# Performance work log

Measured on AMD Instinct MI355X. Metric: run time of the kernel, lower is better.

Reference implementation:

```python
import jax, jax.numpy as jnp
import numpy as np

B, L, D, E, R, NMOD = 8, 2048, 4096, 4, 8, 7

def setup_inputs() -> dict:
    key = jax.random.key(0)
    ks = jax.random.split(key, 8)
    return {
        "x": jax.random.normal(ks[0], (B, L, D), dtype=jnp.float32) * 0.02,
        "expert_scores": jax.random.uniform(ks[1], (B, E), dtype=jnp.float32),
        "W_base": jax.random.normal(ks[2], (D, D), dtype=jnp.float32) * 0.02,
        "b_base": jnp.zeros((D,), dtype=jnp.float32),
        "gating_W": jax.random.normal(ks[3], (D, D), dtype=jnp.float32) * 0.02,
        "W_r": jax.random.normal(ks[4], (NMOD, D), dtype=jnp.float32) * 0.02,
        "lora_A": jax.random.normal(ks[5], (E, R, D), dtype=jnp.float32) * 0.02,
        "lora_B": jax.random.normal(ks[6], (E, D, R), dtype=jnp.float32) * 0.02,
        "module_idx": 0,
        "k": 2,
    }

def _gate_weights(expert_scores, module_prob, k, dtype):
    # rank experts by their random score (descending); Top-K -> weight 1/K
    order = jnp.argsort(-expert_scores, axis=-1)           # [B, E]
    rank = jnp.argsort(order, axis=-1)                     # [B, E] rank of each expert
    k_lo = max(1, k // 2)
    w_hi = (rank < k).astype(dtype) / k                    # prob > 0.5 branch
    w_lo = (rank < k_lo).astype(dtype) / k_lo              # prob <= 0.5 branch
    return jnp.where((module_prob > 0.5)[:, None], w_hi, w_lo)  # [B, E]

def reference(x, expert_scores, W_base, b_base, gating_W, W_r, lora_A, lora_B, module_idx, k):
    # Pooler: last token representation
    pooled = x[:, -1, :]                                   # [B, D]
    # Router: softmax(g(h) W_r) -> per-module probability
    gated = pooled @ gating_W.T                            # [B, D]
    logits = gated @ W_r.T                                 # [B, NMOD]
    probs = jax.nn.softmax(logits, axis=-1)
    module_prob = probs[:, module_idx]                     # [B]
    gate = _gate_weights(expert_scores, module_prob, k, x.dtype)  # [B, E]
    # Base linear projection
    base = x @ W_base.T + b_base                           # [B, L, D]
    # LoRA experts: sum_e gate[b,e] * (x @ A_e^T) @ B_e^T
    t = jnp.einsum('bli,eri->belr', x, lora_A)             # [B, E, L, R]
    lora = jnp.einsum('belr,eor,be->blo', t, lora_B, gate) # [B, L, D]
    return base + lora
```

## Files before the change

### kernel.cpp

```cpp
#include <hip/hip_runtime.h>
#include <hip/hip_bf16.h>


typedef short short8 __attribute__((ext_vector_type(8)));
typedef float f32x4v __attribute__((ext_vector_type(4)));

#define M_DIM 16384
#define N_DIM 4096
#define K_DIM 4160
#define D_DIM 4096
#define NGRP 130

__device__ __forceinline__ unsigned short f2b(float f) {
  unsigned u = __builtin_bit_cast(unsigned, f);
  return (unsigned short)((u + 0x7FFFu + ((u >> 16) & 1u)) >> 16);
}
__device__ __forceinline__ void async_copy16(void* lds, const void* g) {
  __builtin_amdgcn_global_load_lds(
      (const __attribute__((address_space(1))) void*)g,
      (__attribute__((address_space(3))) void*)lds, 16, 0, 0);
}
__device__ __forceinline__ short8 frag_ld(const short* base, int row, int ks, int hi, int lo) {
  return *(const short8*)(&base[row * 64 + (((ks * 4 + hi) ^ (lo & 7)) * 8)]);
}

__global__ __launch_bounds__(256) void cvt_x_k(const float* __restrict__ x,
                                               short* __restrict__ xa) {
  size_t idx = (size_t)blockIdx.x * 256 + threadIdx.x;
  size_t row = idx / 520;
  int cc = (int)(idx % 520);
  short8 o;
  if (cc < 512) {
    const float* src = x + row * (size_t)D_DIM + (size_t)cc * 8;
    float4 a = *(const float4*)(src);
    float4 b = *(const float4*)(src + 4);
    o[0] = (short)f2b(a.x); o[1] = (short)f2b(a.y);
    o[2] = (short)f2b(a.z); o[3] = (short)f2b(a.w);
    o[4] = (short)f2b(b.x); o[5] = (short)f2b(b.y);
    o[6] = (short)f2b(b.z); o[7] = (short)f2b(b.w);
  } else {
#pragma unroll
    for (int t = 0; t < 8; ++t) o[t] = 0;
  }
  *(short8*)(xa + row * (size_t)K_DIM + (size_t)cc * 8) = o;
}

__global__ __launch_bounds__(256) void cvt_w_k(const float* __restrict__ Wb,
                                               const float* __restrict__ lB,
                                               short* __restrict__ wa) {
  size_t idx = (size_t)blockIdx.x * 256 + threadIdx.x;
  size_t row = idx / 520;
  int cc = (int)(idx % 520);
  short8 o;
  if (cc < 512) {
    const float* src = Wb + row * (size_t)D_DIM + (size_t)cc * 8;
    float4 a = *(const float4*)(src);
    float4 b = *(const float4*)(src + 4);
    o[0] = (short)f2b(a.x); o[1] = (short)f2b(a.y);
    o[2] = (short)f2b(a.z); o[3] = (short)f2b(a.w);
    o[4] = (short)f2b(b.x); o[5] = (short)f2b(b.y);
    o[6] = (short)f2b(b.z); o[7] = (short)f2b(b.w);
  } else if (cc < 516) {
    int e = cc - 512;
    const float* src = lB + (size_t)e * (D_DIM * 8) + row * 8;
    float4 a = *(const float4*)(src);
    float4 b = *(const float4*)(src + 4);
    o[0] = (short)f2b(a.x); o[1] = (short)f2b(a.y);
    o[2] = (short)f2b(a.z); o[3] = (short)f2b(a.w);
    o[4] = (short)f2b(b.x); o[5] = (short)f2b(b.y);
    o[6] = (short)f2b(b.z); o[7] = (short)f2b(b.w);
  } else {
#pragma unroll
    for (int t = 0; t < 8; ++t) o[t] = 0;
  }
  *(short8*)(wa + row * (size_t)K_DIM + (size_t)cc * 8) = o;
}

__global__ __launch_bounds__(256) void cvt_la_k(const float* __restrict__ lA,
                                                short* __restrict__ lAb) {
  size_t i = (size_t)blockIdx.x * 256 + threadIdx.x;
  const float* s = lA + i * 8;
  float4 a = *(const float4*)s;
  float4 b = *(const float4*)(s + 4);
  short8 o;
  o[0] = (short)f2b(a.x); o[1] = (short)f2b(a.y);
  o[2] = (short)f2b(a.z); o[3] = (short)f2b(a.w);
  o[4] = (short)f2b(b.x); o[5] = (short)f2b(b.y);
  o[6] = (short)f2b(b.z); o[7] = (short)f2b(b.w);
  *(short8*)(lAb + i * 8) = o;
}

__global__ __launch_bounds__(256) void gated_k(const float* __restrict__ x,
                                               const float* __restrict__ gW,
                                               float* __restrict__ gated) {
  const int j = blockIdx.x;
  const int tid = threadIdx.x;
  float acc[8];
#pragma unroll
  for (int b = 0; b < 8; ++b) acc[b] = 0.f;
  const float* w = gW + (size_t)j * D_DIM;
  for (int i = tid * 4; i < D_DIM; i += 1024) {
    float4 wv = *(const float4*)(w + i);
#pragma unroll
    for (int b = 0; b < 8; ++b) {
      const float* p = x + ((size_t)b * 2048 + 2047) * D_DIM + i;
      float4 pv = *(const float4*)p;
      acc[b] += wv.x * pv.x + wv.y * pv.y + wv.z * pv.z + wv.w * pv.w;
    }
  }
  __shared__ float red[8][4];
  const int lane = tid & 63, wv_ = tid >> 6;
#pragma unroll
  for (int b = 0; b < 8; ++b) {
    float v = acc[b];
    v += __shfl_down(v, 32); v += __shfl_down(v, 16); v += __shfl_down(v, 8);
    v += __shfl_down(v, 4);  v += __shfl_down(v, 2);  v += __shfl_down(v, 1);
    if (lane == 0) red[b][wv_] = v;
  }
  __syncthreads();
  if (tid < 8)
    gated[(size_t)tid * D_DIM + j] = red[tid][0] + red[tid][1] + red[tid][2] + red[tid][3];
}

__global__ void gate_k(const float* __restrict__ gated, const float* __restrict__ Wr,
                       const float* __restrict__ scores, const int* __restrict__ midx_p,
                       const int* __restrict__ kp, float* __restrict__ gate) {
  const int lane = threadIdx.x;
  float acc[56];
#pragma unroll
  for (int t = 0; t < 56; ++t) acc[t] = 0.f;
  for (int i = lane * 4; i < D_DIM; i += 256) {
    float4 g[8]; float4 w[7];
#pragma unroll
    for (int b = 0; b < 8; ++b) g[b] = *(const float4*)(gated + (size_t)b * D_DIM + i);
#pragma unroll
    for (int m = 0; m < 7; ++m) w[m] = *(const float4*)(Wr + (size_t)m * D_DIM + i);
#pragma unroll
    for (int m = 0; m < 7; ++m)
#pragma unroll
      for (int b = 0; b < 8; ++b)
        acc[m * 8 + b] += w[m].x * g[b].x + w[m].y * g[b].y + w[m].z * g[b].z + w[m].w * g[b].w;
  }
  __shared__ float Ls[56];
#pragma unroll
  for (int t = 0; t < 56; ++t) {
    float v = acc[t];
    v += __shfl_xor(v, 1); v += __shfl_xor(v, 2); v += __shfl_xor(v, 4);
    v += __shfl_xor(v, 8); v += __shfl_xor(v, 16); v += __shfl_xor(v, 32);
    if (lane == t) Ls[t] = v;
  }
  __syncthreads();
  if (lane < 8) {
    const int b = lane;
    float mx = -1e30f;
    for (int m = 0; m < 7; ++m) mx = fmaxf(mx, Ls[m * 8 + b]);
    float s = 0.f;
    for (int m = 0; m < 7; ++m) s += expf(Ls[m * 8 + b] - mx);
    const int mi = midx_p[0];
    const float mp = expf(Ls[mi * 8 + b] - mx) / s;
    int kv = kp[0]; if (kv < 1) kv = 1;
    int klo = kv >> 1; if (klo < 1) klo = 1;
    float sc[4];
#pragma unroll
    for (int e = 0; e < 4; ++e) sc[e] = scores[b * 4 + e];
#pragma unroll
    for (int e = 0; e < 4; ++e) {
      int rank = 0;
#pragma unroll
      for (int e2 = 0; e2 < 4; ++e2)
        rank += (sc[e2] > sc[e] || (sc[e2] == sc[e] && e2 < e)) ? 1 : 0;
      float wv = (mp > 0.5f) ? ((rank < kv) ? 1.0f / (float)kv : 0.f)
                             : ((rank < klo) ? 1.0f / (float)klo : 0.f);
      gate[b * 4 + e] = wv;
    }
  }
}

__global__ __launch_bounds__(256) void lora_t_k(const short* __restrict__ XA,
                                                const short* __restrict__ LAb,
                                                const float* __restrict__ gate,
                                                short* __restrict__ xa_w) {
  __shared__ short As[4096];
  __shared__ short Bs[2048];
  const int tid = threadIdx.x, lane = tid & 63, wave = tid >> 6;
  const int lo = lane & 15, hi = lane >> 4;
  const size_t row0 = (size_t)blockIdx.x * 64;
  const int srow = tid >> 3;
  const int slot = (tid & 7) ^ (srow & 7);
  const short* gA = XA + (row0 + srow) * (size_t)K_DIM + slot * 8;
  const short* gB = LAb + (size_t)srow * D_DIM + slot * 8;
  f32x4v acc[2] = {};

  for (int t = 0; t < 64; ++t) {
    const int kt = t * 64;
    char* la = (char*)As + wave * 1024;
    char* lb = (char*)Bs + wave * 1024;
    async_copy16(la, gA + kt);
    async_copy16(la + 4096, gA + (size_t)32 * K_DIM + kt);
    async_copy16(lb, gB + kt);
    __syncthreads();
    short8 a0 = frag_ld(As, wave * 16 + lo, 0, hi, lo);
    short8 a1 = frag_ld(As, wave * 16 + lo, 1, hi, lo);
    short8 b00 = frag_ld(Bs, lo, 0, hi, lo);
    short8 b01 = frag_ld(Bs, lo, 1, hi, lo);
    short8 b10 = frag_ld(Bs, 16 + lo, 0, hi, lo);
    short8 b11 = frag_ld(Bs, 16 + lo, 1, hi, lo);
    acc[0] = __builtin_amdgcn_mfma_f32_16x16x32_bf16(a0, b00, acc[0], 0, 0, 0);
    acc[0] = __builtin_amdgcn_mfma_f32_16x16x32_bf16(a1, b01, acc[0], 0, 0, 0);
    acc[1] = __builtin_amdgcn_mfma_f32_16x16x32_bf16(a0, b10, acc[1], 0, 0, 0);
    acc[1] = __builtin_amdgcn_mfma_f32_16x16x32_bf16(a1, b11, acc[1], 0, 0, 0);
    __syncthreads();
  }
  const int b = (int)(row0 >> 11);
#pragma unroll
  for (int ni = 0; ni < 2; ++ni) {
    const int col = ni * 16 + lo;
    const float g = gate[b * 4 + (col >> 3)];
#pragma unroll
    for (int j = 0; j < 4; ++j) {
      const size_t r = row0 + wave * 16 + hi * 4 + j;
      xa_w[r * (size_t)K_DIM + 4096 + col] = (short)f2b(acc[ni][j] * g);
    }
  }
}

__global__ __launch_bounds__(512, 2) void gemm_k(const short* __restrict__ A,
                                                 const short* __restrict__ B,
                                                 const float* __restrict__ bias,
                                                 float* __restrict__ C) {
  __shared__ short As[4][8192];
  __shared__ short Bs[4][8192];
  const int tid = threadIdx.x;
  const int lane = tid & 63;
  const int wave = tid >> 6;
  const int wm = wave >> 2;
  const int wn = wave & 3;
  const int lo = lane & 15, hi = lane >> 4;

  const int wg = (blockIdx.x & 7) * 128 + (blockIdx.x >> 3);
  const int brow = wg >> 4;
  const int bcol = wg & 15;

  const int srow = tid >> 2;
  const int schunk = (tid & 3) ^ ((tid >> 3) & 3);
  const short* srcA = A + (size_t)(brow * 256 + srow) * K_DIM + schunk * 8;
  const short* srcB = B + (size_t)(bcol * 256 + srow) * K_DIM + schunk * 8;
  char* ldsA0 = (char*)(&As[0][0]) + wave * 1024;
  char* ldsB0 = (char*)(&Bs[0][0]) + wave * 1024;

  const int csw = (hi ^ ((lo >> 1) & 3)) * 8;
  const int aro = (wm * 128 + lo) * 32 + csw;
  const int bro = (wn * 64 + lo) * 32 + csw;

  float bz[4];
#pragma unroll
  for (int ni = 0; ni < 4; ++ni)
    bz[ni] = bias[bcol * 256 + wn * 64 + ni * 16 + lo];

  f32x4v acc[8][4] = {};

#define STAGE_A(koff, ss)                                                      \
  async_copy16(ldsA0 + (ss) * 16384, srcA + (koff));                           \
  async_copy16(ldsA0 + (ss) * 16384 + 8192, srcA + (size_t)128 * K_DIM + (koff));
#define STAGE_B(koff, ss)                                                      \
  async_copy16(ldsB0 + (ss) * 16384, srcB + (koff));                           \
  async_copy16(ldsB0 + (ss) * 16384 + 8192, srcB + (size_t)128 * K_DIM + (koff));

  STAGE_A(0, 0);  STAGE_B(0, 0);
  STAGE_A(32, 1); STAGE_B(32, 1);
  STAGE_A(64, 2); STAGE_B(64, 2);
  asm volatile("s_waitcnt vmcnt(8)" ::: "memory");
  __builtin_amdgcn_s_barrier();

#pragma unroll 4
  for (int g = 0; g < NGRP; ++g) {
    const int slot = g & 3;
    const int gs = (g <= NGRP - 4) ? (g + 3) : (g - 1);
    const int ss = gs & 3;
    const size_t ko = (size_t)gs * 32;
    const short* Aslot = &As[0][0] + slot * 8192;
    const short* Bslot = &Bs[0][0] + slot * 8192;

    short8 afr[4], afr2[4], bfr[4];
#pragma unroll
    for (int mi = 0; mi < 4; ++mi)
      afr[mi] = *(const short8*)(&Aslot[aro + mi * 512]);
#pragma unroll
    for (int ni = 0; ni < 4; ++ni)
      bfr[ni] = *(const short8*)(&Bslot[bro + ni * 512]);
#pragma unroll
    for (int mi = 0; mi < 4; ++mi)
      afr2[mi] = *(const short8*)(&Aslot[aro + 2048 + mi * 512]);

    __builtin_amdgcn_s_setprio(1);
#pragma unroll
    for (int mi = 0; mi < 4; ++mi)
#pragma unroll
      for (int ni = 0; ni < 4; ++ni)
        acc[mi][ni] = __builtin_amdgcn_mfma_f32_16x16x32_bf16(afr[mi], bfr[ni], acc[mi][ni], 0, 0, 0);
    __builtin_amdgcn_s_setprio(0);

    STAGE_A(ko, ss);
    STAGE_B(ko, ss);

    __builtin_amdgcn_s_setprio(1);
#pragma unroll
    for (int mi = 0; mi < 4; ++mi)
#pragma unroll
      for (int ni = 0; ni < 4; ++ni)
        acc[mi + 4][ni] = __builtin_amdgcn_mfma_f32_16x16x32_bf16(afr2[mi], bfr[ni], acc[mi + 4][ni], 0, 0, 0);
    __builtin_amdgcn_s_setprio(0);

    asm volatile("s_waitcnt vmcnt(8)" ::: "memory");
    __builtin_amdgcn_s_barrier();
  }

#pragma unroll
  for (int mi = 0; mi < 8; ++mi) {
#pragma unroll
    for (int ni = 0; ni < 4; ++ni) {
      const int r0 = brow * 256 + wm * 128 + mi * 16 + hi * 4;
      const int c0 = bcol * 256 + wn * 64 + ni * 16 + lo;
#pragma unroll
      for (int j = 0; j < 4; ++j)
        C[(size_t)(r0 + j) * N_DIM + c0] = acc[mi][ni][j] + bz[ni];
    }
  }
#undef STAGE_A
#undef STAGE_B
}

extern "C" void kernel_launch(void* const* d_in, const int* in_sizes, int n_in,
                              void* d_out, int out_size, void* d_ws, size_t ws_size,
                              hipStream_t stream) {
  const float* x      = (const float*)d_in[0];
  const float* scores = (const float*)d_in[1];
  const float* Wb     = (const float*)d_in[2];
  const float* bb     = (const float*)d_in[3];
  const float* gW     = (const float*)d_in[4];
  const float* Wr     = (const float*)d_in[5];
  const float* lA     = (const float*)d_in[6];
  const float* lB     = (const float*)d_in[7];
  const int*   midx   = (const int*)d_in[8];
  const int*   kk     = (const int*)d_in[9];
  float* out = (float*)d_out;

  char* ws = (char*)d_ws;
  short* xa    = (short*)ws;
  short* wa    = (short*)(ws + 136314880u);
  float* gated = (float*)(ws + 136314880u + 34078720u);
  float* gate  = (float*)(ws + 136314880u + 34078720u + 131072u);
  short* lAb   = (short*)(ws + 136314880u + 34078720u + 131072u + 128u);

  cvt_x_k<<<33280, 256, 0, stream>>>(x, xa);
  cvt_w_k<<<8320, 256, 0, stream>>>(Wb, lB, wa);
  cvt_la_k<<<64, 256, 0, stream>>>(lA, lAb);
  gated_k<<<4096, 256, 0, stream>>>(x, gW, gated);
  gate_k<<<1, 64, 0, stream>>>(gated, Wr, scores, midx, kk, gate);
  lora_t_k<<<256, 256, 0, stream>>>(xa, lAb, gate, xa);
  gemm_k<<<1024, 512, 0, stream>>>(xa, wa, bb, out);
}
```

Baseline: 720.9 us.

## Use five-slot LDS ring to process two k-groups per barrier in GEMM

Grows the LDS ring buffer for the A and B tiles from four slots to five. The main loop now handles two k-groups per iteration with a single wait and barrier, keeping a prefetch distance of three groups. The goal is to halve the number of workgroup barriers and waits across the K loop so the MFMA stream stalls less. In exchange, LDS use per block rises to 160KB and the loop body gets larger, with more complex slot indexing.

```diff
diff --git a/kernel.cpp b/kernel.cpp
--- a/kernel.cpp
+++ b/kernel.cpp
@@ -228,8 +228,8 @@
                                                  const short* __restrict__ B,
                                                  const float* __restrict__ bias,
                                                  float* __restrict__ C) {
-  __shared__ short As[4][8192];
-  __shared__ short Bs[4][8192];
+  __shared__ short As[5][8192];
+  __shared__ short Bs[5][8192];
   const int tid = threadIdx.x;
   const int lane = tid & 63;
   const int wave = tid >> 6;
@@ -266,54 +266,63 @@
   async_copy16(ldsB0 + (ss) * 16384, srcB + (koff));                           \
   async_copy16(ldsB0 + (ss) * 16384 + 8192, srcB + (size_t)128 * K_DIM + (koff));
 
+#define GROUP(s, ko, sw)                                                       \
+  {                                                                            \
+    const short* Aslot = &As[0][0] + (s) * 8192;                               \
+    const short* Bslot = &Bs[0][0] + (s) * 8192;                               \
+    short8 afr[4], afr2[4], bfr[4];                                            \
+    _Pragma("unroll")                                                          \
+    for (int mi = 0; mi < 4; ++mi)                                             \
+      afr[mi] = *(const short8*)(&Aslot[aro + mi * 512]);                      \
+    _Pragma("unroll")                                                          \
+    for (int ni = 0; ni < 4; ++ni)                                             \
+      bfr[ni] = *(const short8*)(&Bslot[bro + ni * 512]);                      \
+    _Pragma("unroll")                                                          \
+    for (int mi = 0; mi < 4; ++mi)                                             \
+      afr2[mi] = *(const short8*)(&Aslot[aro + 2048 + mi * 512]);              \
+    __builtin_amdgcn_s_setprio(1);                                             \
+    _Pragma("unroll")                                                          \
+    for (int mi = 0; mi < 4; ++mi)                                             \
+      _Pragma("unroll")                                                        \
+      for (int ni = 0; ni < 4; ++ni)                                           \
+        acc[mi][ni] = __builtin_amdgcn_mfma_f32_16x16x32_bf16(                 \
+            afr[mi], bfr[ni], acc[mi][ni], 0, 0, 0);                           \
+    __builtin_amdgcn_s_setprio(0);                                             \
+    STAGE_A((ko), (sw));                                                       \
+    STAGE_B((ko), (sw));                                                       \
+    __builtin_amdgcn_s_setprio(1);                                             \
+    _Pragma("unroll")                                                          \
+    for (int mi = 0; mi < 4; ++mi)                                             \
+      _Pragma("unroll")                                                        \
+      for (int ni = 0; ni < 4; ++ni)                                           \
+        acc[mi + 4][ni] = __builtin_amdgcn_mfma_f32_16x16x32_bf16(             \
+            afr2[mi], bfr[ni], acc[mi + 4][ni], 0, 0, 0);                      \
+    __builtin_amdgcn_s_setprio(0);                                             \
+  }
+
   STAGE_A(0, 0);  STAGE_B(0, 0);
   STAGE_A(32, 1); STAGE_B(32, 1);
   STAGE_A(64, 2); STAGE_B(64, 2);
-  asm volatile("s_waitcnt vmcnt(8)" ::: "memory");
+  asm volatile("s_waitcnt vmcnt(4)" ::: "memory");
   __builtin_amdgcn_s_barrier();
 
-#pragma unroll 4
-  for (int g = 0; g < NGRP; ++g) {
-    const int slot = g & 3;
-    const int gs = (g <= NGRP - 4) ? (g + 3) : (g - 1);
-    const int ss = gs & 3;
-    const size_t ko = (size_t)gs * 32;
-    const short* Aslot = &As[0][0] + slot * 8192;
-    const short* Bslot = &Bs[0][0] + slot * 8192;
-
-    short8 afr[4], afr2[4], bfr[4];
-#pragma unroll
-    for (int mi = 0; mi < 4; ++mi)
-      afr[mi] = *(const short8*)(&Aslot[aro + mi * 512]);
-#pragma unroll
-    for (int ni = 0; ni < 4; ++ni)
-      bfr[ni] = *(const short8*)(&Bslot[bro + ni * 512]);
-#pragma unroll
-    for (int mi = 0; mi < 4; ++mi)
-      afr2[mi] = *(const short8*)(&Aslot[aro + 2048 + mi * 512]);
-
-    __builtin_amdgcn_s_setprio(1);
-#pragma unroll
-    for (int mi = 0; mi < 4; ++mi)
-#pragma unroll
-      for (int ni = 0; ni < 4; ++ni)
-        acc[mi][ni] = __builtin_amdgcn_mfma_f32_16x16x32_bf16(afr[mi], bfr[ni], acc[mi][ni], 0, 0, 0);
-    __builtin_amdgcn_s_setprio(0);
-
-    STAGE_A(ko, ss);
-    STAGE_B(ko, ss);
-
-    __builtin_amdgcn_s_setprio(1);
-#pragma unroll
-    for (int mi = 0; mi < 4; ++mi)
-#pragma unroll
-      for (int ni = 0; ni < 4; ++ni)
-        acc[mi + 4][ni] = __builtin_amdgcn_mfma_f32_16x16x32_bf16(afr2[mi], bfr[ni], acc[mi + 4][ni], 0, 0, 0);
-    __builtin_amdgcn_s_setprio(0);
-
-    asm volatile("s_waitcnt vmcnt(8)" ::: "memory");
+  int s0 = 0;
+  for (int p = 0; p < 65; ++p) {
+    const int g0 = 2 * p, g1 = g0 + 1;
+    const int s1  = (s0 + 1 == 5) ? 0 : s0 + 1;
+    const int sw0 = (s0 + 3 >= 5) ? s0 - 2 : s0 + 3;
+    const int sw1 = (sw0 + 1 == 5) ? 0 : sw0 + 1;
+    const size_t ko0 = (size_t)((g0 + 3 <= NGRP - 1) ? g0 + 3 : g0 - 2) * 32;
+    const size_t ko1 = (size_t)((g1 + 3 <= NGRP - 1) ? g1 + 3 : g1 - 2) * 32;
+
+    GROUP(s0, ko0, sw0)
+    GROUP(s1, ko1, sw1)
+
+    asm volatile("s_waitcnt vmcnt(4)" ::: "memory");
     __builtin_amdgcn_s_barrier();
-  }
+    s0 = (s0 + 2 >= 5) ? s0 - 3 : s0 + 2;
+  }
+  asm volatile("s_waitcnt vmcnt(0)" ::: "memory");
 
 #pragma unroll
   for (int mi = 0; mi < 8; ++mi) {
@@ -326,6 +335,7 @@
         C[(size_t)(r0 + j) * N_DIM + c0] = acc[mi][ni][j] + bz[ni];
     }
   }
+#undef GROUP
 #undef STAGE_A
 #undef STAGE_B
 }
```

After: 705.8 us, median of 2. -2.1%, faster.
